# Kernel optimization log

Hardware: AMD Instinct MI355X
Metric: run time of the kernel (lower is better)

## Reference

```python
import jax, jax.numpy as jnp
import numpy as np
from jax import lax

SCALE = 2
K_UP = 5
BN_EPS = 1e-5
DN = ('NCHW', 'OIHW', 'NCHW')


def bn_eval(x, gamma, beta):
    # BatchNorm2d in eval mode with running_mean=0, running_var=1
    s = gamma / jnp.sqrt(1.0 + BN_EPS)
    return x * s[None, :, None, None] + beta[None, :, None, None]


def pixel_shuffle(x, r):
    b, C, h, w = x.shape
    c = C // (r * r)
    x = x.reshape(b, c, r, r, h, w)
    x = x.transpose(0, 1, 4, 2, 5, 3)  # b, c, h, r, w, r
    return x.reshape(b, c, h * r, w * r)


def setup_inputs() -> dict:
    key = jax.random.key(0)
    ks = jax.random.split(key, 3)
    b, c, h, w = 4, 128, 64, 64
    c_mid = 64
    return {
        'X': jax.random.normal(ks[0], (b, c, h, w), dtype=jnp.float32),
        'comp_w': jax.random.normal(ks[1], (c_mid, c, 1, 1), dtype=jnp.float32) * 0.05,
        'comp_g': jnp.ones((c_mid,), jnp.float32),
        'comp_b': jnp.zeros((c_mid,), jnp.float32),
        'enc_w': jax.random.normal(ks[2], ((SCALE * K_UP) ** 2, c_mid, 3, 3), dtype=jnp.float32) * 0.05,
        'enc_g': jnp.ones(((SCALE * K_UP) ** 2,), jnp.float32),
        'enc_b': jnp.zeros(((SCALE * K_UP) ** 2,), jnp.float32),
    }


def reference(X, comp_w, comp_g, comp_b, enc_w, enc_g, enc_b):
    b, c, h, w = X.shape
    h_, w_ = h * SCALE, w * SCALE
    pad = K_UP // 2 * SCALE  # = 4

    # comp: 1x1 conv + BN + SiLU
    W = lax.conv_general_dilated(X, comp_w, (1, 1), [(0, 0), (0, 0)], dimension_numbers=DN)
    W = jax.nn.silu(bn_eval(W, comp_g, comp_b))
    # enc: 3x3 conv (pad 1) + BN, no activation
    W = lax.conv_general_dilated(W, enc_w, (1, 1), [(1, 1), (1, 1)], dimension_numbers=DN)
    W = bn_eval(W, enc_g, enc_b)
    # pixel shuffle -> [b, k_up^2, h_, w_], softmax over kernel dim
    W = pixel_shuffle(W, SCALE)
    W = jax.nn.softmax(W, axis=1)

    # nearest-neighbor upsample of X
    Xu = jnp.repeat(jnp.repeat(X, SCALE, axis=2), SCALE, axis=3)  # [b, c, h_, w_]
    # unfold: kernel k_up, dilation=scale, padding=pad (im2col, channel-major)
    P = lax.conv_general_dilated_patches(
        Xu, (K_UP, K_UP), (1, 1), [(pad, pad), (pad, pad)],
        rhs_dilation=(SCALE, SCALE), dimension_numbers=DN)  # [b, c*k^2, h_, w_]
    P = P.reshape(b, c, K_UP * K_UP, h_, w_)

    return jnp.einsum('bkhw,bckhw->bchw', W, P)
```

## Files before the change

kernel.cpp:

```cpp
#include <hip/hip_runtime.h>
#include <hip/hip_bf16.h>
#include <math.h>

#define Bn   4
#define CIN  128
#define Hh   64
#define Ww   64
#define HW   4096
#define CMID 64
#define KOC  100
#define H2   128
#define W2d  128
#define HW2  16384
#define KUP  5
#define BN_EPS 1e-5f
#define CCH  8

typedef __attribute__((ext_vector_type(4)))  short  short4v;
typedef __attribute__((ext_vector_type(8)))  short  short8v;
typedef __attribute__((ext_vector_type(16))) float  float16v;

__device__ __forceinline__ ushort f2bf(float v) {
    __hip_bfloat16 h = __float2bfloat16(v);
    return *(ushort*)&h;
}

__global__ __launch_bounds__(256) void comp_kernel(
    const float* __restrict__ X,
    const float* __restrict__ cw,
    const float* __restrict__ cg,
    const float* __restrict__ cb,
    const float* __restrict__ ew,
    unsigned* __restrict__ W1b,
    ushort* __restrict__ Abf)
{
    int tid = threadIdx.x;
    if (blockIdx.x < 288) {
        int i   = blockIdx.x * 256 + tid;
        int cm  = i & 63;
        int kop = (i >> 6) & 127;
        int tap = i >> 13;
        float v = (kop < KOC) ? ew[((size_t)(kop * CMID + cm)) * 9 + tap] : 0.f;
        Abf[i] = f2bf(v);
    }

    int gt  = blockIdx.x * 256 + tid;
    int pg  = gt & 1023;
    int cog = (gt >> 10) & 31;
    int b   = gt >> 15;
    int pix = pg * 4;
    int co0 = cog * 2;

    const float* xb = X + (size_t)b * CIN * HW + pix;
    float4 acc0 = make_float4(0.f, 0.f, 0.f, 0.f);
    float4 acc1 = make_float4(0.f, 0.f, 0.f, 0.f);

#pragma unroll 4
    for (int ci = 0; ci < CIN; ++ci) {
        float4 xv = *(const float4*)(xb + (size_t)ci * HW);
        float w0 = cw[(size_t)co0 * CIN + ci];
        float w1 = cw[(size_t)(co0 + 1) * CIN + ci];
        acc0.x += xv.x * w0; acc0.y += xv.y * w0; acc0.z += xv.z * w0; acc0.w += xv.w * w0;
        acc1.x += xv.x * w1; acc1.y += xv.y * w1; acc1.z += xv.z * w1; acc1.w += xv.w * w1;
    }

    float inv_s = rsqrtf(1.0f + BN_EPS);
    float s0 = cg[co0] * inv_s,     bb0 = cb[co0];
    float s1 = cg[co0 + 1] * inv_s, bb1 = cb[co0 + 1];
    float r0[4] = {acc0.x, acc0.y, acc0.z, acc0.w};
    float r1[4] = {acc1.x, acc1.y, acc1.z, acc1.w};
#pragma unroll
    for (int i = 0; i < 4; ++i) {
        float v0 = r0[i] * s0 + bb0; v0 = v0 / (1.f + expf(-v0));
        float v1 = r1[i] * s1 + bb1; v1 = v1 / (1.f + expf(-v1));
        unsigned pk = (unsigned)f2bf(v0) | ((unsigned)f2bf(v1) << 16);
        W1b[((size_t)b * HW + pix + i) * 32 + cog] = pk;
    }
}

__global__ __launch_bounds__(256) void enc_kernel(
    const ushort* __restrict__ W1b_us,
    const ushort* __restrict__ Abf,
    float* __restrict__ W2)
{
    __shared__ ushort Bs[3 * 34 * 72];

    int bid   = blockIdx.x;
    int whalf = bid & 1;
    int h     = (bid >> 1) & 63;
    int b     = bid >> 7;
    int w0    = whalf * 32;
    int tid   = threadIdx.x;

    const unsigned* src  = (const unsigned*)W1b_us;
    unsigned*       dstu = (unsigned*)Bs;
    for (int i = tid; i < 3 * 34 * 32; i += 256) {
        int cp = i & 31;
        int t  = i >> 5;
        int wl = t % 34;
        int r  = t / 34;
        int gr = h - 1 + r, gw = w0 - 1 + wl;
        unsigned val = 0u;
        if ((unsigned)gr < 64u && (unsigned)gw < 64u)
            val = src[((size_t)b * HW + gr * 64 + gw) * 32 + cp];
        dstu[(r * 34 + wl) * 36 + cp] = val;
    }
    __syncthreads();

    int lane = tid & 63;
    int wid  = tid >> 6;
    int n    = lane & 31;
    int q    = lane >> 5;

    float16v acc;
#pragma unroll
    for (int i = 0; i < 16; ++i) acc[i] = 0.f;

    const ushort* Arow = Abf + ((size_t)(wid * 32 + n)) * 64 + q * 8;

#pragma unroll
    for (int tap = 0; tap < 9; ++tap) {
        int dy = tap / 3, dx = tap % 3;
        int bbase = ((dy * 34) + n + dx) * 72 + q * 8;
        const ushort* Atap = Arow + (size_t)tap * 128 * 64;
#pragma unroll
        for (int c = 0; c < 4; ++c) {
            short8v a = *(const short8v*)(Atap + c * 16);
            short8v bf = *(const short8v*)(Bs + bbase + c * 16);
            acc = __builtin_amdgcn_mfma_f32_32x32x16_bf16(a, bf, acc, 0, 0, 0);
        }
    }

    int pixn = h * 64 + w0 + n;
    float* Wp = W2 + (size_t)b * KOC * HW + pixn;
#pragma unroll
    for (int reg = 0; reg < 16; ++reg) {
        int row = (reg & 3) + 8 * (reg >> 2) + 4 * q;
        int ko  = wid * 32 + row;
        if (ko < KOC) Wp[(size_t)ko * HW] = acc[reg];
    }
}

__global__ __launch_bounds__(256) void softmax_kernel(
    const float* __restrict__ W2,
    float* __restrict__ Wsm,
    const float* __restrict__ eg,
    const float* __restrict__ eb)
{
    int idx = blockIdx.x * blockDim.x + threadIdx.x;
    int pix = idx & (HW - 1);
    int sub = (idx >> 12) & 3;
    int b   = idx >> 14;

    float inv_s = rsqrtf(1.0f + BN_EPS);
    const float* pi = W2  + (size_t)b * KOC * HW + pix;
    float*       po = Wsm + (size_t)b * KOC * HW + pix;
    float v[25];
    float m = -1e30f;
#pragma unroll
    for (int k = 0; k < 25; ++k) {
        int ko = 4 * k + sub;
        v[k] = pi[(size_t)ko * HW] * (eg[ko] * inv_s) + eb[ko];
        m = fmaxf(m, v[k]);
    }
    float sum = 0.f;
#pragma unroll
    for (int k = 0; k < 25; ++k) {
        v[k] = expf(v[k] - m);
        sum += v[k];
    }
    float inv = 1.f / sum;
#pragma unroll
    for (int k = 0; k < 25; ++k)
        po[(size_t)(4 * k + sub) * HW] = v[k] * inv;
}

__global__ __launch_bounds__(256) void carafe_kernel(
    const float* __restrict__ X,
    const float* __restrict__ Wsm,
    float* __restrict__ out)
{
    int gt = blockIdx.x * blockDim.x + threadIdx.x;
    int w  = gt & 63;
    int h  = (gt >> 6) & 63;
    int b  = (gt >> 12) & 3;
    int chunk = gt >> 14;
    int c0 = chunk * CCH;
    int pix = h * Ww + w;

    float wt[100];
    const float* wpb = Wsm + (size_t)b * KOC * HW + pix;
#pragma unroll
    for (int k = 0; k < 25; ++k) {
        wt[k]      = wpb[(size_t)(4 * k + 0) * HW];
        wt[25 + k] = wpb[(size_t)(4 * k + 1) * HW];
        wt[50 + k] = wpb[(size_t)(4 * k + 2) * HW];
        wt[75 + k] = wpb[(size_t)(4 * k + 3) * HW];
    }

    int off[25];
#pragma unroll
    for (int ki = 0; ki < 5; ++ki) {
#pragma unroll
        for (int kj = 0; kj < 5; ++kj) {
            int k = ki * 5 + kj;
            int r = h + ki - 2, cc = w + kj - 2;
            bool valid = ((unsigned)r < 64u) && ((unsigned)cc < 64u);
            int rc = r < 0 ? 0 : (r > 63 ? 63 : r);
            int cx = cc < 0 ? 0 : (cc > 63 ? 63 : cc);
            off[k] = rc * Ww + cx;
            if (!valid) { wt[k] = 0.f; wt[25+k] = 0.f; wt[50+k] = 0.f; wt[75+k] = 0.f; }
        }
    }

    const float* xp = X + ((size_t)b * CIN + c0) * HW;
    float* o0 = out + ((size_t)b * CIN + c0) * HW2 + (2 * h) * W2d + 2 * w;

    for (int c = 0; c < CCH; ++c) {
        float x[25];
#pragma unroll
        for (int k = 0; k < 25; ++k) x[k] = xp[off[k]];
        float a0 = 0.f, a1 = 0.f, a2 = 0.f, a3 = 0.f;
#pragma unroll
        for (int k = 0; k < 25; ++k) {
            float xv = x[k];
            a0 += wt[k]      * xv;
            a1 += wt[25 + k] * xv;
            a2 += wt[50 + k] * xv;
            a3 += wt[75 + k] * xv;
        }
        *(float2*)o0          = make_float2(a0, a1);
        *(float2*)(o0 + W2d)  = make_float2(a2, a3);
        xp += HW;
        o0 += HW2;
    }
}

extern "C" void kernel_launch(void* const* d_in, const int* in_sizes, int n_in,
                              void* d_out, int out_size, void* d_ws, size_t ws_size,
                              hipStream_t stream)
{
    const float* X  = (const float*)d_in[0];
    const float* cw = (const float*)d_in[1];
    const float* cg = (const float*)d_in[2];
    const float* cb = (const float*)d_in[3];
    const float* ew = (const float*)d_in[4];
    const float* eg = (const float*)d_in[5];
    const float* eb = (const float*)d_in[6];
    float* out = (float*)d_out;

    char* ws = (char*)d_ws;
    unsigned* W1b = (unsigned*)ws;
    ushort*   Abf = (ushort*)(ws + 2097152);
    float*    W2  = (float*)(ws + 2097152 + 147456);
    float*    Wsm = W2 + (size_t)Bn * KOC * HW;

    comp_kernel   <<<512, 256, 0, stream>>>(X, cw, cg, cb, ew, W1b, Abf);
    enc_kernel    <<<512, 256, 0, stream>>>((const ushort*)W1b, Abf, W2);
    softmax_kernel<<<Bn * 4 * HW / 256, 256, 0, stream>>>(W2, Wsm, eg, eb);
    carafe_kernel <<<16 * Bn * HW / 256, 256, 0, stream>>>(X, Wsm, out);
}
```

Before: 129.2 us.

## Fuse softmax into CARAFE kernel via shared memory and rebalance comp tiling

Removes the separate softmax kernel. Each CARAFE block (one row, half-width) now computes the BN+softmax weights for its 32 pixels into shared memory, then 8 thread groups each process 16 channels, reusing those weights. This drops the Wsm write/read round trip and one launch, at the cost of half the threads idling during the softmax phase and fewer blocks (512 vs 1024). The comp kernel is also retiled to compute 4 output channels by 2 pixels per thread instead of 2 by 4.

After: 136.3 us. +5.5%, slower.

```diff
diff --git a/kernel.cpp b/kernel.cpp
--- a/kernel.cpp
+++ b/kernel.cpp
@@ -14,9 +14,7 @@
 #define HW2  16384
 #define KUP  5
 #define BN_EPS 1e-5f
-#define CCH  8
-
-typedef __attribute__((ext_vector_type(4)))  short  short4v;
+
 typedef __attribute__((ext_vector_type(8)))  short  short8v;
 typedef __attribute__((ext_vector_type(16))) float  float16v;
 
@@ -45,36 +43,48 @@
     }
 
     int gt  = blockIdx.x * 256 + tid;
-    int pg  = gt & 1023;
-    int cog = (gt >> 10) & 31;
+    int pg  = gt & 2047;
+    int cog = (gt >> 11) & 15;
     int b   = gt >> 15;
-    int pix = pg * 4;
-    int co0 = cog * 2;
+    int pix = pg * 2;
+    int co0 = cog * 4;
 
     const float* xb = X + (size_t)b * CIN * HW + pix;
-    float4 acc0 = make_float4(0.f, 0.f, 0.f, 0.f);
-    float4 acc1 = make_float4(0.f, 0.f, 0.f, 0.f);
+    float acc[4][2];
+#pragma unroll
+    for (int g = 0; g < 4; ++g) { acc[g][0] = 0.f; acc[g][1] = 0.f; }
 
 #pragma unroll 4
     for (int ci = 0; ci < CIN; ++ci) {
-        float4 xv = *(const float4*)(xb + (size_t)ci * HW);
-        float w0 = cw[(size_t)co0 * CIN + ci];
-        float w1 = cw[(size_t)(co0 + 1) * CIN + ci];
-        acc0.x += xv.x * w0; acc0.y += xv.y * w0; acc0.z += xv.z * w0; acc0.w += xv.w * w0;
-        acc1.x += xv.x * w1; acc1.y += xv.y * w1; acc1.z += xv.z * w1; acc1.w += xv.w * w1;
+        float2 xv = *(const float2*)(xb + (size_t)ci * HW);
+#pragma unroll
+        for (int g = 0; g < 4; ++g) {
+            float wv = cw[(size_t)(co0 + g) * CIN + ci];
+            acc[g][0] += xv.x * wv;
+            acc[g][1] += xv.y * wv;
+        }
     }
 
     float inv_s = rsqrtf(1.0f + BN_EPS);
-    float s0 = cg[co0] * inv_s,     bb0 = cb[co0];
-    float s1 = cg[co0 + 1] * inv_s, bb1 = cb[co0 + 1];
-    float r0[4] = {acc0.x, acc0.y, acc0.z, acc0.w};
-    float r1[4] = {acc1.x, acc1.y, acc1.z, acc1.w};
-#pragma unroll
-    for (int i = 0; i < 4; ++i) {
-        float v0 = r0[i] * s0 + bb0; v0 = v0 / (1.f + expf(-v0));
-        float v1 = r1[i] * s1 + bb1; v1 = v1 / (1.f + expf(-v1));
-        unsigned pk = (unsigned)f2bf(v0) | ((unsigned)f2bf(v1) << 16);
-        W1b[((size_t)b * HW + pix + i) * 32 + cog] = pk;
+    ushort r[4][2];
+#pragma unroll
+    for (int g = 0; g < 4; ++g) {
+        float s  = cg[co0 + g] * inv_s;
+        float bb = cb[co0 + g];
+#pragma unroll
+        for (int i = 0; i < 2; ++i) {
+            float v = acc[g][i] * s + bb;
+            v = v / (1.f + expf(-v));
+            r[g][i] = f2bf(v);
+        }
+    }
+#pragma unroll
+    for (int i = 0; i < 2; ++i) {
+        unsigned lo = (unsigned)r[0][i] | ((unsigned)r[1][i] << 16);
+        unsigned hi = (unsigned)r[2][i] | ((unsigned)r[3][i] << 16);
+        unsigned* dst = W1b + ((size_t)b * HW + pix + i) * 32 + cog * 2;
+        dst[0] = lo;
+        dst[1] = hi;
     }
 }
 
@@ -141,62 +151,59 @@
     }
 }
 
-__global__ __launch_bounds__(256) void softmax_kernel(
-    const float* __restrict__ W2,
-    float* __restrict__ Wsm,
-    const float* __restrict__ eg,
-    const float* __restrict__ eb)
-{
-    int idx = blockIdx.x * blockDim.x + threadIdx.x;
-    int pix = idx & (HW - 1);
-    int sub = (idx >> 12) & 3;
-    int b   = idx >> 14;
-
-    float inv_s = rsqrtf(1.0f + BN_EPS);
-    const float* pi = W2  + (size_t)b * KOC * HW + pix;
-    float*       po = Wsm + (size_t)b * KOC * HW + pix;
-    float v[25];
-    float m = -1e30f;
-#pragma unroll
-    for (int k = 0; k < 25; ++k) {
-        int ko = 4 * k + sub;
-        v[k] = pi[(size_t)ko * HW] * (eg[ko] * inv_s) + eb[ko];
-        m = fmaxf(m, v[k]);
-    }
-    float sum = 0.f;
-#pragma unroll
-    for (int k = 0; k < 25; ++k) {
-        v[k] = expf(v[k] - m);
-        sum += v[k];
-    }
-    float inv = 1.f / sum;
-#pragma unroll
-    for (int k = 0; k < 25; ++k)
-        po[(size_t)(4 * k + sub) * HW] = v[k] * inv;
-}
-
 __global__ __launch_bounds__(256) void carafe_kernel(
     const float* __restrict__ X,
-    const float* __restrict__ Wsm,
+    const float* __restrict__ W2,
+    const float* __restrict__ eg,
+    const float* __restrict__ eb,
     float* __restrict__ out)
 {
-    int gt = blockIdx.x * blockDim.x + threadIdx.x;
-    int w  = gt & 63;
-    int h  = (gt >> 6) & 63;
-    int b  = (gt >> 12) & 3;
-    int chunk = gt >> 14;
-    int c0 = chunk * CCH;
-    int pix = h * Ww + w;
+    __shared__ float wsm[4][25][32];
+
+    int bid   = blockIdx.x;
+    int whalf = bid & 1;
+    int h     = (bid >> 1) & 63;
+    int b     = bid >> 7;
+    int w0    = whalf * 32;
+    int tid   = threadIdx.x;
+
+    if (tid < 128) {
+        int px  = tid & 31;
+        int sub = tid >> 5;
+        float inv_s = rsqrtf(1.0f + BN_EPS);
+        const float* pi = W2 + (size_t)b * KOC * HW + h * 64 + w0 + px;
+        float v[25];
+        float m = -1e30f;
+#pragma unroll
+        for (int k = 0; k < 25; ++k) {
+            int ko = 4 * k + sub;
+            v[k] = pi[(size_t)ko * HW] * (eg[ko] * inv_s) + eb[ko];
+            m = fmaxf(m, v[k]);
+        }
+        float sum = 0.f;
+#pragma unroll
+        for (int k = 0; k < 25; ++k) {
+            v[k] = expf(v[k] - m);
+            sum += v[k];
+        }
+        float inv = 1.f / sum;
+#pragma unroll
+        for (int k = 0; k < 25; ++k)
+            wsm[sub][k][px] = v[k] * inv;
+    }
+    __syncthreads();
+
+    int px  = tid & 31;
+    int grp = tid >> 5;
+    int w   = w0 + px;
+    int c0  = grp * 16;
 
     float wt[100];
-    const float* wpb = Wsm + (size_t)b * KOC * HW + pix;
-#pragma unroll
-    for (int k = 0; k < 25; ++k) {
-        wt[k]      = wpb[(size_t)(4 * k + 0) * HW];
-        wt[25 + k] = wpb[(size_t)(4 * k + 1) * HW];
-        wt[50 + k] = wpb[(size_t)(4 * k + 2) * HW];
-        wt[75 + k] = wpb[(size_t)(4 * k + 3) * HW];
-    }
+#pragma unroll
+    for (int sub = 0; sub < 4; ++sub)
+#pragma unroll
+        for (int k = 0; k < 25; ++k)
+            wt[sub * 25 + k] = wsm[sub][k][px];
 
     int off[25];
 #pragma unroll
@@ -216,7 +223,7 @@
     const float* xp = X + ((size_t)b * CIN + c0) * HW;
     float* o0 = out + ((size_t)b * CIN + c0) * HW2 + (2 * h) * W2d + 2 * w;
 
-    for (int c = 0; c < CCH; ++c) {
+    for (int c = 0; c < 16; ++c) {
         float x[25];
 #pragma unroll
         for (int k = 0; k < 25; ++k) x[k] = xp[off[k]];
@@ -253,10 +260,8 @@
     unsigned* W1b = (unsigned*)ws;
     ushort*   Abf = (ushort*)(ws + 2097152);
     float*    W2  = (float*)(ws + 2097152 + 147456);
-    float*    Wsm = W2 + (size_t)Bn * KOC * HW;
-
-    comp_kernel   <<<512, 256, 0, stream>>>(X, cw, cg, cb, ew, W1b, Abf);
-    enc_kernel    <<<512, 256, 0, stream>>>((const ushort*)W1b, Abf, W2);
-    softmax_kernel<<<Bn * 4 * HW / 256, 256, 0, stream>>>(W2, Wsm, eg, eb);
-    carafe_kernel <<<16 * Bn * HW / 256, 256, 0, stream>>>(X, Wsm, out);
-}
+
+    comp_kernel  <<<512, 256, 0, stream>>>(X, cw, cg, cb, ew, W1b, Abf);
+    enc_kernel   <<<512, 256, 0, stream>>>((const ushort*)W1b, Abf, W2);
+    carafe_kernel<<<512, 256, 0, stream>>>(X, W2, eg, eb, out);
+}
```

## Fuse BN+softmax into enc kernel and stage CARAFE weights in LDS

Applied to the files above, without the earlier changes.

The enc kernel now writes its MFMA accumulators into shared memory and applies BN and softmax there before storing normalized weights. This removes the separate softmax launch and the global round trip of the raw encoder output. The CARAFE kernel is reorganized so each block covers one row-half, loads its 100x32 weight tile into LDS once with coalesced reads, and has each thread handle 16 channels instead of 8. Only half the enc threads do softmax work, and the CARAFE grid drops to 512 blocks, which reduces parallelism.

Measured after the change: 137.6 us. 6.5% more time.

```diff
diff --git a/kernel.cpp b/kernel.cpp
--- a/kernel.cpp
+++ b/kernel.cpp
@@ -14,9 +14,7 @@
 #define HW2  16384
 #define KUP  5
 #define BN_EPS 1e-5f
-#define CCH  8
-
-typedef __attribute__((ext_vector_type(4)))  short  short4v;
+
 typedef __attribute__((ext_vector_type(8)))  short  short8v;
 typedef __attribute__((ext_vector_type(16))) float  float16v;
 
@@ -81,9 +79,12 @@
 __global__ __launch_bounds__(256) void enc_kernel(
     const ushort* __restrict__ W1b_us,
     const ushort* __restrict__ Abf,
-    float* __restrict__ W2)
-{
-    __shared__ ushort Bs[3 * 34 * 72];
+    const float* __restrict__ eg,
+    const float* __restrict__ eb,
+    float* __restrict__ Wsm)
+{
+    __shared__ float lsm[128 * 32];
+    ushort* Bs = (ushort*)lsm;
 
     int bid   = blockIdx.x;
     int whalf = bid & 1;
@@ -131,48 +132,39 @@
         }
     }
 
-    int pixn = h * 64 + w0 + n;
-    float* Wp = W2 + (size_t)b * KOC * HW + pixn;
+    __syncthreads();
+
 #pragma unroll
     for (int reg = 0; reg < 16; ++reg) {
         int row = (reg & 3) + 8 * (reg >> 2) + 4 * q;
-        int ko  = wid * 32 + row;
-        if (ko < KOC) Wp[(size_t)ko * HW] = acc[reg];
-    }
-}
-
-__global__ __launch_bounds__(256) void softmax_kernel(
-    const float* __restrict__ W2,
-    float* __restrict__ Wsm,
-    const float* __restrict__ eg,
-    const float* __restrict__ eb)
-{
-    int idx = blockIdx.x * blockDim.x + threadIdx.x;
-    int pix = idx & (HW - 1);
-    int sub = (idx >> 12) & 3;
-    int b   = idx >> 14;
-
-    float inv_s = rsqrtf(1.0f + BN_EPS);
-    const float* pi = W2  + (size_t)b * KOC * HW + pix;
-    float*       po = Wsm + (size_t)b * KOC * HW + pix;
-    float v[25];
-    float m = -1e30f;
-#pragma unroll
-    for (int k = 0; k < 25; ++k) {
-        int ko = 4 * k + sub;
-        v[k] = pi[(size_t)ko * HW] * (eg[ko] * inv_s) + eb[ko];
-        m = fmaxf(m, v[k]);
-    }
-    float sum = 0.f;
-#pragma unroll
-    for (int k = 0; k < 25; ++k) {
-        v[k] = expf(v[k] - m);
-        sum += v[k];
-    }
-    float inv = 1.f / sum;
-#pragma unroll
-    for (int k = 0; k < 25; ++k)
-        po[(size_t)(4 * k + sub) * HW] = v[k] * inv;
+        lsm[(wid * 32 + row) * 32 + n] = acc[reg];
+    }
+    __syncthreads();
+
+    if (tid < 128) {
+        int px  = tid & 31;
+        int sub = tid >> 5;
+        float inv_s = rsqrtf(1.0f + BN_EPS);
+        float v[25];
+        float m = -1e30f;
+#pragma unroll
+        for (int k = 0; k < 25; ++k) {
+            int ko = 4 * k + sub;
+            v[k] = lsm[ko * 32 + px] * (eg[ko] * inv_s) + eb[ko];
+            m = fmaxf(m, v[k]);
+        }
+        float sum = 0.f;
+#pragma unroll
+        for (int k = 0; k < 25; ++k) {
+            v[k] = expf(v[k] - m);
+            sum += v[k];
+        }
+        float inv = 1.f / sum;
+        float* po = Wsm + (size_t)b * KOC * HW + h * 64 + w0 + px;
+#pragma unroll
+        for (int k = 0; k < 25; ++k)
+            po[(size_t)(4 * k + sub) * HW] = v[k] * inv;
+    }
 }
 
 __global__ __launch_bounds__(256) void carafe_kernel(
@@ -180,23 +172,34 @@
     const float* __restrict__ Wsm,
     float* __restrict__ out)
 {
-    int gt = blockIdx.x * blockDim.x + threadIdx.x;
-    int w  = gt & 63;
-    int h  = (gt >> 6) & 63;
-    int b  = (gt >> 12) & 3;
-    int chunk = gt >> 14;
-    int c0 = chunk * CCH;
-    int pix = h * Ww + w;
+    __shared__ float wsm[4][25][32];
+
+    int bid   = blockIdx.x;
+    int whalf = bid & 1;
+    int h     = (bid >> 1) & 63;
+    int b     = bid >> 7;
+    int w0    = whalf * 32;
+    int tid   = threadIdx.x;
+
+    const float* wsrc = Wsm + (size_t)b * KOC * HW + h * 64 + w0;
+    for (int i = tid; i < 3200; i += 256) {
+        int px = i & 31;
+        int ko = i >> 5;
+        wsm[ko & 3][ko >> 2][px] = wsrc[(size_t)ko * HW + px];
+    }
+    __syncthreads();
+
+    int px  = tid & 31;
+    int grp = tid >> 5;
+    int w   = w0 + px;
+    int c0  = grp * 16;
 
     float wt[100];
-    const float* wpb = Wsm + (size_t)b * KOC * HW + pix;
-#pragma unroll
-    for (int k = 0; k < 25; ++k) {
-        wt[k]      = wpb[(size_t)(4 * k + 0) * HW];
-        wt[25 + k] = wpb[(size_t)(4 * k + 1) * HW];
-        wt[50 + k] = wpb[(size_t)(4 * k + 2) * HW];
-        wt[75 + k] = wpb[(size_t)(4 * k + 3) * HW];
-    }
+#pragma unroll
+    for (int sub = 0; sub < 4; ++sub)
+#pragma unroll
+        for (int k = 0; k < 25; ++k)
+            wt[sub * 25 + k] = wsm[sub][k][px];
 
     int off[25];
 #pragma unroll
@@ -216,7 +219,7 @@
     const float* xp = X + ((size_t)b * CIN + c0) * HW;
     float* o0 = out + ((size_t)b * CIN + c0) * HW2 + (2 * h) * W2d + 2 * w;
 
-    for (int c = 0; c < CCH; ++c) {
+    for (int c = 0; c < 16; ++c) {
         float x[25];
 #pragma unroll
         for (int k = 0; k < 25; ++k) x[k] = xp[off[k]];
@@ -252,11 +255,9 @@
     char* ws = (char*)d_ws;
     unsigned* W1b = (unsigned*)ws;
     ushort*   Abf = (ushort*)(ws + 2097152);
-    float*    W2  = (float*)(ws + 2097152 + 147456);
-    float*    Wsm = W2 + (size_t)Bn * KOC * HW;
-
-    comp_kernel   <<<512, 256, 0, stream>>>(X, cw, cg, cb, ew, W1b, Abf);
-    enc_kernel    <<<512, 256, 0, stream>>>((const ushort*)W1b, Abf, W2);
-    softmax_kernel<<<Bn * 4 * HW / 256, 256, 0, stream>>>(W2, Wsm, eg, eb);
-    carafe_kernel <<<16 * Bn * HW / 256, 256, 0, stream>>>(X, Wsm, out);
-}
+    float*    Wsm = (float*)(ws + 2097152 + 147456);
+
+    comp_kernel  <<<512, 256, 0, stream>>>(X, cw, cg, cb, ew, W1b, Abf);
+    enc_kernel   <<<512, 256, 0, stream>>>((const ushort*)W1b, Abf, eg, eb, Wsm);
+    carafe_kernel<<<512, 256, 0, stream>>>(X, Wsm, out);
+}
```
